# Kernel optimization log

Hardware: AMD Instinct MI355X
Metric: run time of the kernel (lower is better)

## Reference

```python
import jax, jax.numpy as jnp
import numpy as np

N = 32768   # total nodes
P = 1024    # nodes per graph
B = 32      # graphs (N = B*P)
D = 256     # dim_h
H = 8       # num_heads
E = 262144  # edges
BN_EPS = 1e-5


def setup_inputs() -> dict:
    key = jax.random.key(0)
    ks = jax.random.split(key, 24)
    s = 0.05
    x = jax.random.normal(ks[0], (N, D), jnp.float32)
    src = jax.random.randint(ks[1], (E,), 0, N, dtype=jnp.int32)
    dst = (src // P) * P + jax.random.randint(ks[2], (E,), 0, P, dtype=jnp.int32)
    edge_index = jnp.stack([src, dst])  # [2, E], edges within the same graph
    edge_attr = jax.random.normal(ks[3], (E, D), jnp.float32)
    return {
        "x": x,
        "edge_index": edge_index,
        "edge_attr": edge_attr,
        # GINE nn: Linear(D,D) -> ReLU -> Linear(D,D)
        "gin_w1": s * jax.random.normal(ks[4], (D, D)),
        "gin_b1": jnp.zeros((D,)),
        "gin_w2": s * jax.random.normal(ks[5], (D, D)),
        "gin_b2": jnp.zeros((D,)),
        # MultiheadAttention packed in-proj and out-proj
        "in_w": s * jax.random.normal(ks[6], (3 * D, D)),
        "in_b": jnp.zeros((3 * D,)),
        "out_w": s * jax.random.normal(ks[7], (D, D)),
        "out_b": jnp.zeros((D,)),
        # BatchNorm1d affine params (training-mode batch stats)
        "bn1l_g": jnp.ones((D,)) + s * jax.random.normal(ks[8], (D,)),
        "bn1l_b": s * jax.random.normal(ks[9], (D,)),
        "bn1a_g": jnp.ones((D,)) + s * jax.random.normal(ks[10], (D,)),
        "bn1a_b": s * jax.random.normal(ks[11], (D,)),
        # FF block: Linear(D,2D) -> ReLU -> Linear(2D,D)
        "ff_w1": s * jax.random.normal(ks[12], (2 * D, D)),
        "ff_b1": jnp.zeros((2 * D,)),
        "ff_w2": s * jax.random.normal(ks[13], (D, 2 * D)),
        "ff_b2": jnp.zeros((D,)),
        "bn2_g": jnp.ones((D,)) + s * jax.random.normal(ks[14], (D,)),
        "bn2_b": s * jax.random.normal(ks[15], (D,)),
    }


def _batchnorm(x, g, b):
    # BatchNorm1d, training mode: biased batch statistics over the node axis.
    m = jnp.mean(x, axis=0)
    v = jnp.mean((x - m) ** 2, axis=0)
    return g * (x - m) * jax.lax.rsqrt(v + BN_EPS) + b


def reference(x, edge_index, edge_attr, gin_w1, gin_b1, gin_w2, gin_b2,
              in_w, in_b, out_w, out_b, bn1l_g, bn1l_b, bn1a_g, bn1a_b,
              ff_w1, ff_b1, ff_w2, ff_b2, bn2_g, bn2_b):
    h_in = x
    # ---- local branch: GINEConv (eps = 0) ----
    msg = jax.nn.relu(x[edge_index[0]] + edge_attr)          # [E, D]
    aggr = jax.ops.segment_sum(msg, edge_index[1], num_segments=N)
    z = x + aggr                                             # (1+eps)*x_i + sum msg
    h_local = jax.nn.relu(z @ gin_w1.T + gin_b1) @ gin_w2.T + gin_b2
    h_local = _batchnorm(h_in + h_local, bn1l_g, bn1l_b)
    # ---- global branch: dense-batch MHA (equal-size graphs -> full mask) ----
    hd = x.reshape(B, P, D)
    qkv = hd @ in_w.T + in_b                                 # [B, P, 3D]
    q, k, v = jnp.split(qkv, 3, axis=-1)
    dh = D // H
    q = q.reshape(B, P, H, dh).transpose(0, 2, 1, 3)         # [B, H, P, dh]
    k = k.reshape(B, P, H, dh).transpose(0, 2, 1, 3)
    v = v.reshape(B, P, H, dh).transpose(0, 2, 1, 3)
    scores = jnp.einsum("bhqd,bhkd->bhqk", q, k) / np.sqrt(dh)
    attn = jax.nn.softmax(scores, axis=-1)
    o = jnp.einsum("bhqk,bhkd->bhqd", attn, v)               # [B, H, P, dh]
    o = o.transpose(0, 2, 1, 3).reshape(B, P, D) @ out_w.T + out_b
    h_attn = o.reshape(N, D)
    h_attn = _batchnorm(h_in + h_attn, bn1a_g, bn1a_b)
    # ---- combine + FF + norm ----
    h = h_local + h_attn
    ff = jax.nn.relu(h @ ff_w1.T + ff_b1) @ ff_w2.T + ff_b2
    h = _batchnorm(h + ff, bn2_g, bn2_b)
    return h
```

## Files before the change

### kernel.cpp

```cpp
#include <hip/hip_runtime.h>
#include <hip/hip_bf16.h>

constexpr int D = 256;
constexpr int PG = 1024;

typedef __attribute__((ext_vector_type(8))) short bf16x8;
typedef __attribute__((ext_vector_type(4))) float f32x4;

__device__ inline short f2bf(float f) {
    __hip_bfloat16 h = __float2bfloat16(f);
    return *reinterpret_cast<short*>(&h);
}
__device__ inline float bf2f(short s) {
    return __uint_as_float(((unsigned)(unsigned short)s) << 16);
}
__device__ inline void gl_lds16(const short* g, short* s) {
    __builtin_amdgcn_global_load_lds(
        (const __attribute__((address_space(1))) void*)g,
        (__attribute__((address_space(3))) void*)s, 16, 0, 0);
}

__global__ __launch_bounds__(256) void cvt_bf16(
    const float* __restrict__ X, short* __restrict__ Y)
{
    int i = blockIdx.x * 256 + threadIdx.x;
    float4 a = ((const float4*)X)[i * 2];
    float4 b = ((const float4*)X)[i * 2 + 1];
    bf16x8 v;
    v[0] = f2bf(a.x); v[1] = f2bf(a.y); v[2] = f2bf(a.z); v[3] = f2bf(a.w);
    v[4] = f2bf(b.x); v[5] = f2bf(b.y); v[6] = f2bf(b.z); v[7] = f2bf(b.w);
    ((bf16x8*)Y)[i] = v;
}

__global__ __launch_bounds__(256) void cvt_weights(
    const float* __restrict__ w1, const float* __restrict__ w2,
    const float* __restrict__ w3, const float* __restrict__ w4,
    const float* __restrict__ w5, const float* __restrict__ w6,
    short* __restrict__ out)
{
    int i = blockIdx.x * 256 + threadIdx.x;
    const float* src; int base;
    if (i < 16384)      { if (i < 8192) { src = w1; base = 0; }
                          else          { src = w2; base = 8192; } }
    else if (i < 40960) { src = w3; base = 16384; }
    else if (i < 49152) { src = w4; base = 40960; }
    else if (i < 65536) { src = w5; base = 49152; }
    else                { src = w6; base = 65536; }
    int k = i - base;
    float4 a = ((const float4*)src)[k * 2];
    float4 b = ((const float4*)src)[k * 2 + 1];
    bf16x8 v;
    v[0] = f2bf(a.x); v[1] = f2bf(a.y); v[2] = f2bf(a.z); v[3] = f2bf(a.w);
    v[4] = f2bf(b.x); v[5] = f2bf(b.y); v[6] = f2bf(b.z); v[7] = f2bf(b.w);
    ((bf16x8*)out)[i] = v;
}

__global__ __launch_bounds__(256) void hist_kernel(
    const int* __restrict__ dst, int* __restrict__ cnt, int E)
{
    int e = blockIdx.x * 256 + threadIdx.x;
    if (e < E) atomicAdd(&cnt[dst[e]], 1);
}

__global__ __launch_bounds__(256) void scan_block(
    const int* __restrict__ cnt, int* __restrict__ excl, int* __restrict__ bsum)
{
    __shared__ int sm[256];
    const int t = threadIdx.x;
    const int i = blockIdx.x * 256 + t;
    int v = cnt[i];
    sm[t] = v;
    __syncthreads();
    #pragma unroll
    for (int o = 1; o < 256; o <<= 1) {
        int u = (t >= o) ? sm[t - o] : 0;
        __syncthreads();
        sm[t] += u;
        __syncthreads();
    }
    excl[i] = sm[t] - v;
    if (t == 255) bsum[blockIdx.x] = sm[255];
}

__global__ __launch_bounds__(128) void scan_bsum(int* __restrict__ bsum)
{
    __shared__ int sm[128];
    const int t = threadIdx.x;
    int v = bsum[t];
    sm[t] = v;
    __syncthreads();
    #pragma unroll
    for (int o = 1; o < 128; o <<= 1) {
        int u = (t >= o) ? sm[t - o] : 0;
        __syncthreads();
        sm[t] += u;
        __syncthreads();
    }
    bsum[t] = sm[t] - v;
}

__global__ __launch_bounds__(256) void scan_add(
    const int* __restrict__ excl, const int* __restrict__ bsum,
    int* __restrict__ rowptr, int* __restrict__ ofs)
{
    int i = blockIdx.x * 256 + threadIdx.x;
    int r = excl[i] + bsum[blockIdx.x];
    rowptr[i] = r;
    ofs[i] = r;
}

__global__ __launch_bounds__(256) void scatter_kernel(
    const int* __restrict__ src, const int* __restrict__ dst,
    int* __restrict__ ofs, int* __restrict__ eord, int* __restrict__ esrc, int E)
{
    int e = blockIdx.x * 256 + threadIdx.x;
    if (e >= E) return;
    int d = dst[e];
    int pos = atomicAdd(&ofs[d], 1);
    eord[pos] = e;
    esrc[pos] = src[e];
}

__global__ __launch_bounds__(256) void csr_aggr(
    const float* __restrict__ x, const float* __restrict__ ea,
    const int* __restrict__ rowptr, const int* __restrict__ cnt,
    const int* __restrict__ eord, const int* __restrict__ esrc,
    short* __restrict__ z)
{
    int gid = blockIdx.x * 256 + threadIdx.x;
    int node = gid >> 6;
    int c = (gid & 63) << 2;
    int start = rowptr[node];
    int deg = cnt[node];
    float4 acc = *(const float4*)(x + (size_t)node * D + c);
    for (int i = 0; i < deg; ++i) {
        int e = eord[start + i];
        int s = esrc[start + i];
        float4 xa = *(const float4*)(x + (size_t)s * D + c);
        float4 av = *(const float4*)(ea + (size_t)e * D + c);
        acc.x += fmaxf(xa.x + av.x, 0.f);
        acc.y += fmaxf(xa.y + av.y, 0.f);
        acc.z += fmaxf(xa.z + av.z, 0.f);
        acc.w += fmaxf(xa.w + av.w, 0.f);
    }
    short4 r;
    r.x = f2bf(acc.x); r.y = f2bf(acc.y); r.z = f2bf(acc.z); r.w = f2bf(acc.w);
    *(short4*)(z + (size_t)node * D + c) = r;
}

template<bool RELU, bool ADDF, bool ADDB, bool STATS, bool SCALEQ>
__global__ __launch_bounds__(256) void gemm_mfma(
    const short* __restrict__ X, const short* __restrict__ W,
    const float* __restrict__ bias,
    const float* __restrict__ addf, const short* __restrict__ addb,
    short* __restrict__ Y, float* __restrict__ st, int K, int M)
{
    __shared__ __align__(16) short Xs[128 * 64];
    __shared__ __align__(16) short Ws[128 * 64];

    const int nbx = gridDim.x;
    const int nwg = nbx * gridDim.y;
    const int bid = blockIdx.y * nbx + blockIdx.x;
    const int cpx = nwg >> 3;
    const int wg  = (bid & 7) * cpx + (bid >> 3);
    const int r0 = (wg / nbx) * 128;
    const int c0 = (wg % nbx) * 128;

    const int t = threadIdx.x, w = t >> 6, l = t & 63;
    const int wr = w >> 1, wc = w & 1, lg = l >> 4, lm = l & 15;
    const int srl = l >> 3;
    const int scol = (l & 7) * 8;

    f32x4 acc[4][4];
    #pragma unroll
    for (int i = 0; i < 4; ++i)
        #pragma unroll
        for (int j = 0; j < 4; ++j)
            acc[i][j] = (f32x4){0.f, 0.f, 0.f, 0.f};

    for (int k0 = 0; k0 < K; k0 += 64) {
        __syncthreads();
        #pragma unroll
        for (int it = 0; it < 4; ++it) {
            int r = w * 32 + it * 8;
            gl_lds16(X + (size_t)(r0 + r + srl) * K + k0 + scol, &Xs[r * 64]);
            gl_lds16(W + (size_t)(c0 + r + srl) * K + k0 + scol, &Ws[r * 64]);
        }
        __syncthreads();

        bf16x8 af[4][2], bfr[4][2];
        #pragma unroll
        for (int i = 0; i < 4; ++i)
            #pragma unroll
            for (int ks = 0; ks < 2; ++ks) {
                af[i][ks]  = *(const bf16x8*)&Xs[(wr*64 + i*16 + lm)*64 + ks*32 + lg*8];
                bfr[i][ks] = *(const bf16x8*)&Ws[(wc*64 + i*16 + lm)*64 + ks*32 + lg*8];
            }
        #pragma unroll
        for (int i = 0; i < 4; ++i)
            #pragma unroll
            for (int j = 0; j < 4; ++j) {
                acc[i][j] = __builtin_amdgcn_mfma_f32_16x16x32_bf16(af[i][0], bfr[j][0], acc[i][j], 0, 0, 0);
                acc[i][j] = __builtin_amdgcn_mfma_f32_16x16x32_bf16(af[i][1], bfr[j][1], acc[i][j], 0, 0, 0);
            }
    }

    float s4[4] = {}, q4[4] = {};
    #pragma unroll
    for (int j = 0; j < 4; ++j) {
        int col = c0 + wc*64 + j*16 + lm;
        float bj = bias[col];
        #pragma unroll
        for (int i = 0; i < 4; ++i) {
            #pragma unroll
            for (int r = 0; r < 4; ++r) {
                int row = r0 + wr*64 + i*16 + lg*4 + r;
                size_t off = (size_t)row * M + col;
                float v = acc[i][j][r] + bj;
                if (RELU) v = fmaxf(v, 0.f);
                if (SCALEQ) { if (col < 256) v *= 0.17677669529663687f; }
                if (ADDF) v += addf[off];
                if (ADDB) v += bf2f(addb[off]);
                if (STATS) { s4[j] += v; q4[j] = fmaf(v, v, q4[j]); }
                Y[off] = f2bf(v);
            }
        }
    }
    if (STATS) {
        #pragma unroll
        for (int j = 0; j < 4; ++j) {
            s4[j] += __shfl_xor(s4[j], 16); q4[j] += __shfl_xor(q4[j], 16);
            s4[j] += __shfl_xor(s4[j], 32); q4[j] += __shfl_xor(q4[j], 32);
        }
        if (lg == 0) {
            #pragma unroll
            for (int j = 0; j < 4; ++j) {
                int col = c0 + wc*64 + j*16 + lm;
                atomicAdd(&st[col], s4[j]);
                atomicAdd(&st[256 + col], q4[j]);
            }
        }
    }
}

__global__ __launch_bounds__(256) void attn_mfma(
    const short* __restrict__ QKV, short* __restrict__ O)
{
    const int bh = blockIdx.x & 255;
    const int qblk = blockIdx.x >> 8;
    const int b = bh >> 3, h = bh & 7;
    const int t = threadIdx.x, w = t >> 6, l = t & 63;
    const int lg = l >> 4, lm = l & 15;
    const size_t gb = (size_t)b * PG * 768;
    const int q0 = qblk * 128 + w * 32;

    __shared__ __align__(16) short Ks[64 * 40];
    __shared__ __align__(16) short Vt[32 * 72];
    __shared__ __align__(16) short Ps[4][32 * 72];

    bf16x8 qa[2];
    #pragma unroll
    for (int qt = 0; qt < 2; ++qt)
        qa[qt] = *(const bf16x8*)(QKV + gb + (size_t)(q0 + qt*16 + lm) * 768 + h*32 + lg*8);

    f32x4 acc[2][2];
    #pragma unroll
    for (int qt = 0; qt < 2; ++qt)
        #pragma unroll
        for (int hf = 0; hf < 2; ++hf)
            acc[qt][hf] = (f32x4){0.f, 0.f, 0.f, 0.f};
    float lsum[2] = {0.f, 0.f};

    const int srow = t >> 2;
    const int sq = (t & 3) * 8;
    const short* Kb = QKV + gb + 256 + h*32 + sq;
    const short* Vb = QKV + gb + 512 + h*32 + sq;

    bf16x8 kreg = *(const bf16x8*)(Kb + (size_t)srow * 768);
    bf16x8 vreg = *(const bf16x8*)(Vb + (size_t)srow * 768);

    for (int kt = 0; kt < 16; ++kt) {
        *(bf16x8*)&Ks[srow * 40 + sq] = kreg;
        #pragma unroll
        for (int j = 0; j < 8; ++j) Vt[(sq + j) * 72 + srow] = vreg[j];
        __syncthreads();
        if (kt < 15) {
            kreg = *(const bf16x8*)(Kb + (size_t)((kt + 1) * 64 + srow) * 768);
            vreg = *(const bf16x8*)(Vb + (size_t)((kt + 1) * 64 + srow) * 768);
        }

        bf16x8 kf[4];
        #pragma unroll
        for (int s = 0; s < 4; ++s)
            kf[s] = *(const bf16x8*)&Ks[(s*16 + lm) * 40 + lg*8];

        #pragma unroll
        for (int qt = 0; qt < 2; ++qt) {
            #pragma unroll
            for (int s = 0; s < 4; ++s) {
                f32x4 c = (f32x4){0.f, 0.f, 0.f, 0.f};
                c = __builtin_amdgcn_mfma_f32_16x16x32_bf16(kf[s], qa[qt], c, 0, 0, 0);
                float p0 = __expf(c[0]), p1 = __expf(c[1]);
                float p2 = __expf(c[2]), p3 = __expf(c[3]);
                lsum[qt] += (p0 + p1) + (p2 + p3);
                short4 pk;
                pk.x = f2bf(p0); pk.y = f2bf(p1); pk.z = f2bf(p2); pk.w = f2bf(p3);
                *(short4*)&Ps[w][(qt*16 + lm) * 72 + s*16 + lg*4] = pk;
            }
        }

        bf16x8 vf[2][2];
        #pragma unroll
        for (int hf = 0; hf < 2; ++hf)
            #pragma unroll
            for (int g = 0; g < 2; ++g)
                vf[hf][g] = *(const bf16x8*)&Vt[(hf*16 + lm) * 72 + g*32 + lg*8];
        #pragma unroll
        for (int qt = 0; qt < 2; ++qt) {
            #pragma unroll
            for (int g = 0; g < 2; ++g) {
                bf16x8 pf = *(const bf16x8*)&Ps[w][(qt*16 + lm) * 72 + g*32 + lg*8];
                #pragma unroll
                for (int hf = 0; hf < 2; ++hf)
                    acc[qt][hf] = __builtin_amdgcn_mfma_f32_16x16x32_bf16(
                        pf, vf[hf][g], acc[qt][hf], 0, 0, 0);
            }
        }
        __syncthreads();
    }

    float red[2];
    #pragma unroll
    for (int qt = 0; qt < 2; ++qt) {
        float v = lsum[qt];
        v += __shfl_xor(v, 16);
        v += __shfl_xor(v, 32);
        red[qt] = 1.0f / v;
    }
    #pragma unroll
    for (int qt = 0; qt < 2; ++qt) {
        #pragma unroll
        for (int r = 0; r < 4; ++r) {
            float inv = __shfl(red[qt], lg*4 + r);
            int qrow = q0 + qt*16 + lg*4 + r;
            short* Op = O + ((size_t)b * PG + qrow) * D + h * 32;
            Op[lm]      = f2bf(acc[qt][0][r] * inv);
            Op[16 + lm] = f2bf(acc[qt][1][r] * inv);
        }
    }
}

__global__ __launch_bounds__(256) void bn_combine(
    const short* __restrict__ A, const short* __restrict__ Bq,
    const float* __restrict__ gl, const float* __restrict__ bl,
    const float* __restrict__ ga, const float* __restrict__ ba,
    const float* __restrict__ st, short* __restrict__ H, int n)
{
    const float invN = 1.0f / (float)n;
    size_t i = (size_t)blockIdx.x * 256 + threadIdx.x;
    int c0 = (int)((i & 31) << 3);
    bf16x8 av = ((const bf16x8*)A)[i];
    bf16x8 bv = ((const bf16x8*)Bq)[i];
    bf16x8 o;
    #pragma unroll
    for (int e = 0; e < 8; ++e) {
        int c = c0 + e;
        float m1 = st[c] * invN;
        float v1 = fmaxf(st[256 + c] * invN - m1 * m1, 0.f);
        float m2 = st[512 + c] * invN;
        float v2 = fmaxf(st[768 + c] * invN - m2 * m2, 0.f);
        float y1 = gl[c] * (bf2f(av[e]) - m1) * rsqrtf(v1 + 1e-5f) + bl[c];
        float y2 = ga[c] * (bf2f(bv[e]) - m2) * rsqrtf(v2 + 1e-5f) + ba[c];
        o[e] = f2bf(y1 + y2);
    }
    ((bf16x8*)H)[i] = o;
}

__global__ __launch_bounds__(256) void bn_apply(
    const short* __restrict__ X, const float* __restrict__ g,
    const float* __restrict__ bb, const float* __restrict__ st,
    float* __restrict__ out, int n)
{
    const float invN = 1.0f / (float)n;
    size_t i = (size_t)blockIdx.x * 256 + threadIdx.x;
    int c0 = (int)((i & 31) << 3);
    bf16x8 xv = ((const bf16x8*)X)[i];
    float r[8];
    #pragma unroll
    for (int e = 0; e < 8; ++e) {
        int c = c0 + e;
        float m = st[c] * invN;
        float v = fmaxf(st[256 + c] * invN - m * m, 0.f);
        r[e] = g[c] * (bf2f(xv[e]) - m) * rsqrtf(v + 1e-5f) + bb[c];
    }
    float4 o0 = {r[0], r[1], r[2], r[3]};
    float4 o1 = {r[4], r[5], r[6], r[7]};
    ((float4*)out)[i * 2]     = o0;
    ((float4*)out)[i * 2 + 1] = o1;
}

extern "C" void kernel_launch(void* const* d_in, const int* in_sizes, int n_in,
                              void* d_out, int out_size, void* d_ws, size_t ws_size,
                              hipStream_t stream)
{
    const float* x    = (const float*)d_in[0];
    const int*   ei   = (const int*)d_in[1];
    const float* ea   = (const float*)d_in[2];
    const float* gw1  = (const float*)d_in[3];
    const float* gb1  = (const float*)d_in[4];
    const float* gw2  = (const float*)d_in[5];
    const float* gb2  = (const float*)d_in[6];
    const float* inw  = (const float*)d_in[7];
    const float* inb  = (const float*)d_in[8];
    const float* outw = (const float*)d_in[9];
    const float* outb = (const float*)d_in[10];
    const float* g1l  = (const float*)d_in[11];
    const float* b1l  = (const float*)d_in[12];
    const float* g1a  = (const float*)d_in[13];
    const float* b1a  = (const float*)d_in[14];
    const float* fw1  = (const float*)d_in[15];
    const float* fb1  = (const float*)d_in[16];
    const float* fw2  = (const float*)d_in[17];
    const float* fb2  = (const float*)d_in[18];
    const float* g2   = (const float*)d_in[19];
    const float* b2   = (const float*)d_in[20];
    float* out = (float*)d_out;

    const int N = in_sizes[0] / D;
    const int E = in_sizes[1] / 2;
    const size_t ND = (size_t)N * D;

    short* Bp = (short*)d_ws;
    short* S0 = Bp;
    short* S1 = Bp + ND;
    short* S2 = Bp + 2 * ND;
    short* S3 = Bp + 3 * ND;
    short* S4 = Bp + 4 * ND;
    short* Wb = Bp + 5 * ND;
    short* gw1b = Wb, *gw2b = Wb + 65536, *inwb = Wb + 131072;
    short* outwb = Wb + 327680, *fw1b = Wb + 393216, *fw2b = Wb + 524288;
    float* st = (float*)(Wb + 655360);
    int* cnt    = (int*)(st + 1536);
    int* excl   = cnt + N;
    int* rowptr = excl + N;
    int* ofs    = rowptr + N;
    int* bsum   = ofs + N;
    int* eord   = bsum + 256;
    int* esrc   = eord + E;
    short* xb   = (short*)(esrc + E);

    const int GR = N / 128;
    const int EB = (E + 255) / 256;

    cvt_bf16<<<(unsigned)(ND / 8 / 256), 256, 0, stream>>>(x, xb);
    cvt_weights<<<320, 256, 0, stream>>>(gw1, gw2, inw, outw, fw1, fw2, Wb);

    hipMemsetAsync(st, 0, (1536 + (size_t)N) * sizeof(int), stream);
    hist_kernel<<<EB, 256, 0, stream>>>(ei + E, cnt, E);
    scan_block<<<N / 256, 256, 0, stream>>>(cnt, excl, bsum);
    scan_bsum<<<1, 128, 0, stream>>>(bsum);
    scan_add<<<N / 256, 256, 0, stream>>>(excl, bsum, rowptr, ofs);
    scatter_kernel<<<EB, 256, 0, stream>>>(ei, ei + E, ofs, eord, esrc, E);

    csr_aggr<<<(N * 64) / 256, 256, 0, stream>>>(x, ea, rowptr, cnt, eord, esrc, S0);
    gemm_mfma<true , false, false, false, false><<<dim3(2, GR), 256, 0, stream>>>(
        S0, gw1b, gb1, nullptr, nullptr, S1, nullptr, 256, 256);
    gemm_mfma<false, true , false, true , false><<<dim3(2, GR), 256, 0, stream>>>(
        S1, gw2b, gb2, x, nullptr, S3, st, 256, 256);

    gemm_mfma<false, false, false, false, true ><<<dim3(6, GR), 256, 0, stream>>>(
        xb, inwb, inb, nullptr, nullptr, S0, nullptr, 256, 768);
    attn_mfma<<<(N / PG) * 8 * 8, 256, 0, stream>>>(S0, S4);
    gemm_mfma<false, true , false, true , false><<<dim3(2, GR), 256, 0, stream>>>(
        S4, outwb, outb, x, nullptr, S0, st + 512, 256, 256);

    bn_combine<<<(unsigned)(ND / 8 / 256), 256, 0, stream>>>(
        S3, S0, g1l, b1l, g1a, b1a, st, S1, N);
    gemm_mfma<true , false, false, false, false><<<dim3(4, GR), 256, 0, stream>>>(
        S1, fw1b, fb1, nullptr, nullptr, S2, nullptr, 256, 512);
    gemm_mfma<false, false, true , true , false><<<dim3(2, GR), 256, 0, stream>>>(
        S2, fw2b, fb2, nullptr, S1, S4, st + 1024, 512, 256);
    bn_apply<<<(unsigned)(ND / 8 / 256), 256, 0, stream>>>(
        S4, g2, b2, st + 1024, out, N);
}
```

Baseline: 403.9 us.

## Fuse independent local and global branch kernels into shared launches

Merges the independent GINE branch and attention branch stages into combined kernels that dispatch work by block index: conversion plus histogram in one launch, CSR aggregation interleaved with the QKV GEMM, GIN GEMM1 interleaved with attention, and both stat-producing GEMMs in one launch. The goal is to cut launch count and let memory-bound and compute-bound work run concurrently on the GPU. In exchange, shared memory is sized to the largest user in every fused kernel, which may lower occupancy for the lighter parts. The interleave ratios are hardcoded to the problem's block counts.

```diff
diff --git a/kernel.cpp b/kernel.cpp
--- a/kernel.cpp
+++ b/kernel.cpp
@@ -20,10 +20,10 @@
         (__attribute__((address_space(3))) void*)s, 16, 0, 0);
 }
 
-__global__ __launch_bounds__(256) void cvt_bf16(
-    const float* __restrict__ X, short* __restrict__ Y)
-{
-    int i = blockIdx.x * 256 + threadIdx.x;
+__device__ __forceinline__ void cvt_bf16_body(
+    int bid, const float* __restrict__ X, short* __restrict__ Y)
+{
+    int i = bid * 256 + threadIdx.x;
     float4 a = ((const float4*)X)[i * 2];
     float4 b = ((const float4*)X)[i * 2 + 1];
     bf16x8 v;
@@ -32,13 +32,13 @@
     ((bf16x8*)Y)[i] = v;
 }
 
-__global__ __launch_bounds__(256) void cvt_weights(
-    const float* __restrict__ w1, const float* __restrict__ w2,
+__device__ __forceinline__ void cvt_weights_body(
+    int bid, const float* __restrict__ w1, const float* __restrict__ w2,
     const float* __restrict__ w3, const float* __restrict__ w4,
     const float* __restrict__ w5, const float* __restrict__ w6,
     short* __restrict__ out)
 {
-    int i = blockIdx.x * 256 + threadIdx.x;
+    int i = bid * 256 + threadIdx.x;
     const float* src; int base;
     if (i < 16384)      { if (i < 8192) { src = w1; base = 0; }
                           else          { src = w2; base = 8192; } }
@@ -55,79 +55,13 @@
     ((bf16x8*)out)[i] = v;
 }
 
-__global__ __launch_bounds__(256) void hist_kernel(
-    const int* __restrict__ dst, int* __restrict__ cnt, int E)
-{
-    int e = blockIdx.x * 256 + threadIdx.x;
-    if (e < E) atomicAdd(&cnt[dst[e]], 1);
-}
-
-__global__ __launch_bounds__(256) void scan_block(
-    const int* __restrict__ cnt, int* __restrict__ excl, int* __restrict__ bsum)
-{
-    __shared__ int sm[256];
-    const int t = threadIdx.x;
-    const int i = blockIdx.x * 256 + t;
-    int v = cnt[i];
-    sm[t] = v;
-    __syncthreads();
-    #pragma unroll
-    for (int o = 1; o < 256; o <<= 1) {
-        int u = (t >= o) ? sm[t - o] : 0;
-        __syncthreads();
-        sm[t] += u;
-        __syncthreads();
-    }
-    excl[i] = sm[t] - v;
-    if (t == 255) bsum[blockIdx.x] = sm[255];
-}
-
-__global__ __launch_bounds__(128) void scan_bsum(int* __restrict__ bsum)
-{
-    __shared__ int sm[128];
-    const int t = threadIdx.x;
-    int v = bsum[t];
-    sm[t] = v;
-    __syncthreads();
-    #pragma unroll
-    for (int o = 1; o < 128; o <<= 1) {
-        int u = (t >= o) ? sm[t - o] : 0;
-        __syncthreads();
-        sm[t] += u;
-        __syncthreads();
-    }
-    bsum[t] = sm[t] - v;
-}
-
-__global__ __launch_bounds__(256) void scan_add(
-    const int* __restrict__ excl, const int* __restrict__ bsum,
-    int* __restrict__ rowptr, int* __restrict__ ofs)
-{
-    int i = blockIdx.x * 256 + threadIdx.x;
-    int r = excl[i] + bsum[blockIdx.x];
-    rowptr[i] = r;
-    ofs[i] = r;
-}
-
-__global__ __launch_bounds__(256) void scatter_kernel(
-    const int* __restrict__ src, const int* __restrict__ dst,
-    int* __restrict__ ofs, int* __restrict__ eord, int* __restrict__ esrc, int E)
-{
-    int e = blockIdx.x * 256 + threadIdx.x;
-    if (e >= E) return;
-    int d = dst[e];
-    int pos = atomicAdd(&ofs[d], 1);
-    eord[pos] = e;
-    esrc[pos] = src[e];
-}
-
-__global__ __launch_bounds__(256) void csr_aggr(
-    const float* __restrict__ x, const float* __restrict__ ea,
+__device__ __forceinline__ void csr_aggr_body(
+    int bid, const float* __restrict__ x, const float* __restrict__ ea,
     const int* __restrict__ rowptr, const int* __restrict__ cnt,
     const int* __restrict__ eord, const int* __restrict__ esrc,
     short* __restrict__ z)
 {
-    int gid = blockIdx.x * 256 + threadIdx.x;
+    int gid = bid * 256 + threadIdx.x;
     int node = gid >> 6;
     int c = (gid & 63) << 2;
     int start = rowptr[node];
@@ -149,20 +83,19 @@
 }
 
 template<bool RELU, bool ADDF, bool ADDB, bool STATS, bool SCALEQ>
-__global__ __launch_bounds__(256) void gemm_mfma(
+__device__ __forceinline__ void gemm_body(
+    int qid, int nbx, int nwg,
     const short* __restrict__ X, const short* __restrict__ W,
     const float* __restrict__ bias,
     const float* __restrict__ addf, const short* __restrict__ addb,
-    short* __restrict__ Y, float* __restrict__ st, int K, int M)
-{
-    __shared__ __align__(16) short Xs[128 * 64];
-    __shared__ __align__(16) short Ws[128 * 64];
-
-    const int nbx = gridDim.x;
-    const int nwg = nbx * gridDim.y;
-    const int bid = blockIdx.y * nbx + blockIdx.x;
+    short* __restrict__ Y, float* __restrict__ st, int K, int M,
+    short* SM)
+{
+    short* Xs = SM;
+    short* Ws = SM + 8192;
+
     const int cpx = nwg >> 3;
-    const int wg  = (bid & 7) * cpx + (bid >> 3);
+    const int wg  = (qid & 7) * cpx + (qid >> 3);
     const int r0 = (wg / nbx) * 128;
     const int c0 = (wg % nbx) * 128;
 
@@ -243,20 +176,20 @@
     }
 }
 
-__global__ __launch_bounds__(256) void attn_mfma(
-    const short* __restrict__ QKV, short* __restrict__ O)
-{
-    const int bh = blockIdx.x & 255;
-    const int qblk = blockIdx.x >> 8;
+__device__ __forceinline__ void attn_body(
+    int aid, const short* __restrict__ QKV, short* __restrict__ O, short* SM)
+{
+    const int bh = aid & 255;
+    const int qblk = aid >> 8;
     const int b = bh >> 3, h = bh & 7;
     const int t = threadIdx.x, w = t >> 6, l = t & 63;
     const int lg = l >> 4, lm = l & 15;
     const size_t gb = (size_t)b * PG * 768;
     const int q0 = qblk * 128 + w * 32;
 
-    __shared__ __align__(16) short Ks[64 * 40];
-    __shared__ __align__(16) short Vt[32 * 72];
-    __shared__ __align__(16) short Ps[4][32 * 72];
+    short* Ks = SM;
+    short* Vt = SM + 2560;
+    short* Pw = SM + 4864 + w * 2304;
 
     bf16x8 qa[2];
     #pragma unroll
@@ -305,7 +238,7 @@
                 lsum[qt] += (p0 + p1) + (p2 + p3);
                 short4 pk;
                 pk.x = f2bf(p0); pk.y = f2bf(p1); pk.z = f2bf(p2); pk.w = f2bf(p3);
-                *(short4*)&Ps[w][(qt*16 + lm) * 72 + s*16 + lg*4] = pk;
+                *(short4*)&Pw[(qt*16 + lm) * 72 + s*16 + lg*4] = pk;
             }
         }
 
@@ -319,7 +252,7 @@
         for (int qt = 0; qt < 2; ++qt) {
             #pragma unroll
             for (int g = 0; g < 2; ++g) {
-                bf16x8 pf = *(const bf16x8*)&Ps[w][(qt*16 + lm) * 72 + g*32 + lg*8];
+                bf16x8 pf = *(const bf16x8*)&Pw[(qt*16 + lm) * 72 + g*32 + lg*8];
                 #pragma unroll
                 for (int hf = 0; hf < 2; ++hf)
                     acc[qt][hf] = __builtin_amdgcn_mfma_f32_16x16x32_bf16(
@@ -348,6 +281,151 @@
             Op[16 + lm] = f2bf(acc[qt][1][r] * inv);
         }
     }
+}
+
+__global__ __launch_bounds__(256) void fused0(
+    const float* __restrict__ x, short* __restrict__ xb,
+    const float* __restrict__ w1, const float* __restrict__ w2,
+    const float* __restrict__ w3, const float* __restrict__ w4,
+    const float* __restrict__ w5, const float* __restrict__ w6,
+    short* __restrict__ Wb,
+    const int* __restrict__ dst, int* __restrict__ cnt, int E)
+{
+    int bid = blockIdx.x;
+    if (bid < 4096) {
+        cvt_bf16_body(bid, x, xb);
+    } else if (bid < 4416) {
+        cvt_weights_body(bid - 4096, w1, w2, w3, w4, w5, w6, Wb);
+    } else {
+        int e = (bid - 4416) * 256 + threadIdx.x;
+        if (e < E) atomicAdd(&cnt[dst[e]], 1);
+    }
+}
+
+__global__ __launch_bounds__(256) void fusedB(
+    const float* __restrict__ x, const float* __restrict__ ea,
+    const int* __restrict__ rowptr, const int* __restrict__ cnt,
+    const int* __restrict__ eord, const int* __restrict__ esrc,
+    short* __restrict__ Zb,
+    const short* __restrict__ xb, const short* __restrict__ inwb,
+    const float* __restrict__ inb, short* __restrict__ QKVb)
+{
+    __shared__ __align__(16) short SM[16384];
+    int bid = blockIdx.x;
+    int grp = bid / 19, rem = bid % 19;
+    if (rem < 3) {
+        int qid = grp * 3 + rem;
+        gemm_body<false, false, false, false, true>(
+            qid, 6, 1536, xb, inwb, inb, nullptr, nullptr, QKVb, nullptr, 256, 768, SM);
+    } else {
+        csr_aggr_body(grp * 16 + (rem - 3), x, ea, rowptr, cnt, eord, esrc, Zb);
+    }
+}
+
+__global__ __launch_bounds__(256) void fusedC(
+    const short* __restrict__ Zb, const short* __restrict__ gw1b,
+    const float* __restrict__ gb1, short* __restrict__ T1b,
+    const short* __restrict__ QKVb, short* __restrict__ Ob)
+{
+    __shared__ __align__(16) short SM[16384];
+    int bid = blockIdx.x;
+    int grp = bid / 5, rem = bid % 5;
+    if (rem == 0) {
+        gemm_body<true, false, false, false, false>(
+            grp, 2, 512, Zb, gw1b, gb1, nullptr, nullptr, T1b, nullptr, 256, 256, SM);
+    } else {
+        attn_body(grp * 4 + (rem - 1), QKVb, Ob, SM);
+    }
+}
+
+__global__ __launch_bounds__(256) void fusedD(
+    const short* __restrict__ T1b, const short* __restrict__ gw2b,
+    const float* __restrict__ gb2, const float* __restrict__ x,
+    short* __restrict__ F0b,
+    const short* __restrict__ Ob, const short* __restrict__ outwb,
+    const float* __restrict__ outb, short* __restrict__ F1b,
+    float* __restrict__ st)
+{
+    __shared__ __align__(16) short SM[16384];
+    int bid = blockIdx.x;
+    if ((bid & 1) == 0) {
+        gemm_body<false, true, false, true, false>(
+            bid >> 1, 2, 512, T1b, gw2b, gb2, x, nullptr, F0b, st, 256, 256, SM);
+    } else {
+        gemm_body<false, true, false, true, false>(
+            bid >> 1, 2, 512, Ob, outwb, outb, x, nullptr, F1b, st + 512, 256, 256, SM);
+    }
+}
+
+template<bool RELU, bool ADDF, bool ADDB, bool STATS>
+__global__ __launch_bounds__(256) void gemm_k(
+    const short* __restrict__ X, const short* __restrict__ W,
+    const float* __restrict__ bias,
+    const float* __restrict__ addf, const short* __restrict__ addb,
+    short* __restrict__ Y, float* __restrict__ st, int K, int M, int nbx)
+{
+    __shared__ __align__(16) short SM[16384];
+    gemm_body<RELU, ADDF, ADDB, STATS, false>(
+        blockIdx.x, nbx, gridDim.x, X, W, bias, addf, addb, Y, st, K, M, SM);
+}
+
+__global__ __launch_bounds__(256) void scan_block(
+    const int* __restrict__ cnt, int* __restrict__ excl, int* __restrict__ bsum)
+{
+    __shared__ int sm[256];
+    const int t = threadIdx.x;
+    const int i = blockIdx.x * 256 + t;
+    int v = cnt[i];
+    sm[t] = v;
+    __syncthreads();
+    #pragma unroll
+    for (int o = 1; o < 256; o <<= 1) {
+        int u = (t >= o) ? sm[t - o] : 0;
+        __syncthreads();
+        sm[t] += u;
+        __syncthreads();
+    }
+    excl[i] = sm[t] - v;
+    if (t == 255) bsum[blockIdx.x] = sm[255];
+}
+
+__global__ __launch_bounds__(128) void scan_bsum(int* __restrict__ bsum)
+{
+    __shared__ int sm[128];
+    const int t = threadIdx.x;
+    int v = bsum[t];
+    sm[t] = v;
+    __syncthreads();
+    #pragma unroll
+    for (int o = 1; o < 128; o <<= 1) {
+        int u = (t >= o) ? sm[t - o] : 0;
+        __syncthreads();
+        sm[t] += u;
+        __syncthreads();
+    }
+    bsum[t] = sm[t] - v;
+}
+
+__global__ __launch_bounds__(256) void scan_add(
+    const int* __restrict__ excl, const int* __restrict__ bsum,
+    int* __restrict__ rowptr, int* __restrict__ ofs)
+{
+    int i = blockIdx.x * 256 + threadIdx.x;
+    int r = excl[i] + bsum[blockIdx.x];
+    rowptr[i] = r;
+    ofs[i] = r;
+}
+
+__global__ __launch_bounds__(256) void scatter_kernel(
+    const int* __restrict__ src, const int* __restrict__ dst,
+    int* __restrict__ ofs, int* __restrict__ eord, int* __restrict__ esrc, int E)
+{
+    int e = blockIdx.x * 256 + threadIdx.x;
+    if (e >= E) return;
+    int d = dst[e];
+    int pos = atomicAdd(&ofs[d], 1);
+    eord[pos] = e;
+    esrc[pos] = src[e];
 }
 
 __global__ __launch_bounds__(256) void bn_combine(
@@ -431,12 +509,14 @@
     const size_t ND = (size_t)N * D;
 
     short* Bp = (short*)d_ws;
-    short* S0 = Bp;
-    short* S1 = Bp + ND;
-    short* S2 = Bp + 2 * ND;
-    short* S3 = Bp + 3 * ND;
-    short* S4 = Bp + 4 * ND;
-    short* Wb = Bp + 5 * ND;
+    short* A0 = Bp;
+    short* A1 = Bp + ND;
+    short* A2 = Bp + 2 * ND;
+    short* A3 = Bp + 3 * ND;
+    short* A4 = Bp + 4 * ND;
+    short* A5 = Bp + 5 * ND;
+    short* xb = Bp + 6 * ND;
+    short* Wb = Bp + 7 * ND;
     short* gw1b = Wb, *gw2b = Wb + 65536, *inwb = Wb + 131072;
     short* outwb = Wb + 327680, *fw1b = Wb + 393216, *fw2b = Wb + 524288;
     float* st = (float*)(Wb + 655360);
@@ -447,39 +527,32 @@
     int* bsum   = ofs + N;
     int* eord   = bsum + 256;
     int* esrc   = eord + E;
-    short* xb   = (short*)(esrc + E);
-
-    const int GR = N / 128;
+
     const int EB = (E + 255) / 256;
 
-    cvt_bf16<<<(unsigned)(ND / 8 / 256), 256, 0, stream>>>(x, xb);
-    cvt_weights<<<320, 256, 0, stream>>>(gw1, gw2, inw, outw, fw1, fw2, Wb);
-
     hipMemsetAsync(st, 0, (1536 + (size_t)N) * sizeof(int), stream);
-    hist_kernel<<<EB, 256, 0, stream>>>(ei + E, cnt, E);
+    fused0<<<4416 + EB, 256, 0, stream>>>(
+        x, xb, gw1, gw2, inw, outw, fw1, fw2, Wb, ei + E, cnt, E);
+
     scan_block<<<N / 256, 256, 0, stream>>>(cnt, excl, bsum);
     scan_bsum<<<1, 128, 0, stream>>>(bsum);
     scan_add<<<N / 256, 256, 0, stream>>>(excl, bsum, rowptr, ofs);
     scatter_kernel<<<EB, 256, 0, stream>>>(ei, ei + E, ofs, eord, esrc, E);
 
-    csr_aggr<<<(N * 64) / 256, 256, 0, stream>>>(x, ea, rowptr, cnt, eord, esrc, S0);
-    gemm_mfma<true , false, false, false, false><<<dim3(2, GR), 256, 0, stream>>>(
-        S0, gw1b, gb1, nullptr, nullptr, S1, nullptr, 256, 256);
-    gemm_mfma<false, true , false, true , false><<<dim3(2, GR), 256, 0, stream>>>(
-        S1, gw2b, gb2, x, nullptr, S3, st, 256, 256);
-
-    gemm_mfma<false, false, false, false, true ><<<dim3(6, GR), 256, 0, stream>>>(
-        xb, inwb, inb, nullptr, nullptr, S0, nullptr, 256, 768);
-    attn_mfma<<<(N / PG) * 8 * 8, 256, 0, stream>>>(S0, S4);
-    gemm_mfma<false, true , false, true , false><<<dim3(2, GR), 256, 0, stream>>>(
-        S4, outwb, outb, x, nullptr, S0, st + 512, 256, 256);
+    fusedB<<<9728, 256, 0, stream>>>(
+        x, ea, rowptr, cnt, eord, esrc, A0, xb, inwb, inb, A1);
+
+    fusedC<<<2560, 256, 0, stream>>>(A0, gw1b, gb1, A4, A1, A5);
+
+    fusedD<<<1024, 256, 0, stream>>>(
+        A4, gw2b, gb2, x, A0, A5, outwb, outb, A1, st);
 
     bn_combine<<<(unsigned)(ND / 8 / 256), 256, 0, stream>>>(
-        S3, S0, g1l, b1l, g1a, b1a, st, S1, N);
-    gemm_mfma<true , false, false, false, false><<<dim3(4, GR), 256, 0, stream>>>(
-        S1, fw1b, fb1, nullptr, nullptr, S2, nullptr, 256, 512);
-    gemm_mfma<false, false, true , true , false><<<dim3(2, GR), 256, 0, stream>>>(
-        S2, fw2b, fb2, nullptr, S1, S4, st + 1024, 512, 256);
+        A0, A1, g1l, b1l, g1a, b1a, st, A2, N);
+    gemm_k<true , false, false, false><<<1024, 256, 0, stream>>>(
+        A2, fw1b, fb1, nullptr, nullptr, A3, nullptr, 256, 512, 4);
+    gemm_k<false, false, true , true ><<<512, 256, 0, stream>>>(
+        A3, fw2b, fb2, nullptr, A2, A5, st + 1024, 512, 256, 2);
     bn_apply<<<(unsigned)(ND / 8 / 256), 256, 0, stream>>>(
-        S4, g2, b2, st + 1024, out, N);
-}
+        A5, g2, b2, st + 1024, out, N);
+}
```

Result: slower. 432.5 us (+7.1%).
